# Performance work log

Hardware: AMD Instinct MI355X
Metric: run time of the kernel (lower is better)

The kernel has to match this reference:

```python
import jax, jax.numpy as jnp
import numpy as np

SPEED_OF_SOUND = 343.0
SAMPLING_FREQUENCY = 96000.0
REC_LEN = 4096   # recording_length_samples
CROP_LEN = 128   # crop_length_samples
NUM_RECV = 8
B1, B2 = 4, 16384
HIDDEN = 32


def setup_inputs() -> dict:
    key = jax.random.key(0)
    ks = jax.random.split(key, 6)
    recordings = jax.random.normal(ks[0], (B1, NUM_RECV, REC_LEN), dtype=jnp.float32)
    sample_locations = jax.random.normal(ks[1], (B1, B2, 3), dtype=jnp.float32)
    emitter_location = jax.random.normal(ks[2], (3,), dtype=jnp.float32)
    receiver_locations = jax.random.normal(ks[3], (NUM_RECV, 3), dtype=jnp.float32)
    W1 = 0.02 * jax.random.normal(ks[4], (NUM_RECV * CROP_LEN, HIDDEN), dtype=jnp.float32)
    b1 = jnp.zeros((HIDDEN,), dtype=jnp.float32)
    W2 = 0.02 * jax.random.normal(ks[5], (HIDDEN, 1), dtype=jnp.float32)
    b2 = jnp.zeros((1,), dtype=jnp.float32)
    return {
        "recordings": recordings,
        "sample_locations": sample_locations,
        "emitter_location": emitter_location,
        "receiver_locations": receiver_locations,
        "W1": W1, "b1": b1, "W2": W2, "b2": b2,
    }


def reference(recordings, sample_locations, emitter_location, receiver_locations, W1, b1, W2, b2):
    # recordings: (B1, R, L); sample_locations: (B1, B2, 3)
    b1_, R, L = recordings.shape
    b2_ = sample_locations.shape[1]
    K = W1.shape[0] // R  # crop_length_samples

    # time-of-flight distances
    d_emit = jnp.linalg.norm(sample_locations - emitter_location, axis=-1)              # (B1, B2)
    d_recv = jnp.linalg.norm(sample_locations[:, :, None, :] - receiver_locations, axis=-1)  # (B1, B2, R)
    total_samples = jnp.round((d_emit[..., None] + d_recv) / SPEED_OF_SOUND * SAMPLING_FREQUENCY)
    crop_start = total_samples - K // 2                                                  # (B1, B2, R)

    # normalized grid coordinates, exactly as in the torch module
    grid_base = -1.0 + 2.0 * (crop_start / L)                                            # (B1, B2, R)
    grid_offset = jnp.linspace(0.0, 0.5 * (K - 1) / L, K, dtype=jnp.float32)             # (K,)
    gx = grid_base[..., None] + grid_offset                                              # (B1, B2, R, K)

    # Exact torch grid_sample(mode='bilinear', align_corners=False, zero padding) on
    # input of shape (N, 1, H=L, W=1) with grid = (x=gx, y=0). In torch, x indexes the
    # WIDTH dim (size 1) and y=0 indexes the HEIGHT dim (size L), so:
    #   iy = ((0+1)*L - 1)/2 = (L-1)/2  (constant -> blend of the two center samples)
    #   ix = ((gx+1)*1 - 1)/2 = gx/2    (triangle weight around the single width pixel)
    iy = (L - 1) / 2.0
    iy0 = int(np.floor(iy))
    wy1 = jnp.float32(iy - iy0)
    wy0 = jnp.float32(1.0) - wy1
    vy = wy0 * recordings[..., iy0] + wy1 * recordings[..., iy0 + 1]                     # (B1, R)

    ix = gx * 0.5
    ix0 = jnp.floor(ix)
    fx = ix - ix0
    # corner at width index ix0 is in-bounds iff ix0 == 0; corner ix0+1 iff ix0 == -1
    w = (1.0 - fx) * (ix0 == 0.0).astype(ix.dtype) + fx * (ix0 == -1.0).astype(ix.dtype)
    crops = w * vy[:, None, :, None]                                                     # (B1, B2, R, K)

    # tiny MLP head
    x = crops.reshape(b1_ * b2_, R * K)
    h = jax.nn.relu(x @ W1 + b1)
    pred = (h @ W2 + b2).reshape(b1_, b2_)
    return pred
```

## Files before the change

### kernel.cpp

```cpp
#include <hip/hip_runtime.h>
#include <math.h>

#define TMAX 6336
#define B2N  16384

__global__ __launch_bounds__(256) void build_S(const float* __restrict__ W1,
                                               float* __restrict__ S) {
  const int r  = blockIdx.y;
  const int T0 = blockIdx.x * 64;
  __shared__ float W1s[128 * 32];
  __shared__ float wls[128 * 64];
  const int t = threadIdx.x;

  const float4* src = (const float4*)(W1 + r * 128 * 32);
  float4* dst = (float4*)W1s;
#pragma unroll
  for (int i = 0; i < 4; i++) dst[t + i * 256] = src[t + i * 256];

  for (int e = t; e < 128 * 64; e += 256) {
    const int k  = e >> 6;
    const int Tl = e & 63;
    const float g0 = (float)(T0 + Tl - 64) * (1.0f / 2048.0f) - 1.0f;
    const float gx = g0 + (float)k * (1.0f / 8192.0f);
    wls[e] = fmaxf(0.0f, fmaf(-0.5f, fabsf(gx), 1.0f));
  }
  __syncthreads();

  const int h  = t & 31;
  const int tb = t >> 5;
  float acc[8] = {0.f, 0.f, 0.f, 0.f, 0.f, 0.f, 0.f, 0.f};
#pragma unroll 4
  for (int k = 0; k < 128; k++) {
    const float wv = W1s[k * 32 + h];
    const float4* wp = (const float4*)(&wls[k * 64 + tb * 8]);
    const float4 w0 = wp[0];
    const float4 w1 = wp[1];
    acc[0] = fmaf(w0.x, wv, acc[0]);
    acc[1] = fmaf(w0.y, wv, acc[1]);
    acc[2] = fmaf(w0.z, wv, acc[2]);
    acc[3] = fmaf(w0.w, wv, acc[3]);
    acc[4] = fmaf(w1.x, wv, acc[4]);
    acc[5] = fmaf(w1.y, wv, acc[5]);
    acc[6] = fmaf(w1.z, wv, acc[6]);
    acc[7] = fmaf(w1.w, wv, acc[7]);
  }
#pragma unroll
  for (int j = 0; j < 8; j++) {
    const int T = T0 + tb * 8 + j;
    S[(((T << 3) + r) << 5) + h] = acc[j];
  }
}

__global__ __launch_bounds__(256) void tof_main(
    const float* __restrict__ recordings, const float* __restrict__ sloc,
    const float* __restrict__ emit, const float* __restrict__ rloc,
    const float* __restrict__ b1v, const float* __restrict__ W2,
    const float* __restrict__ b2v, const float* __restrict__ S,
    float* __restrict__ out) {
  __shared__ float vy[8];
  __shared__ float em[3];
  __shared__ float rl[24];
  __shared__ float b1s[32];
  __shared__ float W2s[32];
  __shared__ float b2s;
  const int t = threadIdx.x;
  const int sid = blockIdx.x * 256 + t;
  const int b = sid >> 14;

  if (t < 8) {
    const float* rp = recordings + ((b << 3) + t) * 4096;
    vy[t] = 0.5f * (rp[2047] + rp[2048]);
  }
  if (t < 3) em[t] = emit[t];
  if (t >= 32 && t < 56) rl[t - 32] = rloc[t - 32];
  if (t >= 64 && t < 96) b1s[t - 64] = b1v[t - 64];
  if (t >= 96 && t < 128) W2s[t - 96] = W2[t - 96];
  if (t == 128) b2s = b2v[0];
  __syncthreads();

  const float x = sloc[sid * 3 + 0];
  const float y = sloc[sid * 3 + 1];
  const float z = sloc[sid * 3 + 2];
  const float ex = x - em[0], ey = y - em[1], ez = z - em[2];
  const float de = sqrtf(ex * ex + ey * ey + ez * ez);

  float acc[32];
#pragma unroll
  for (int h = 0; h < 32; h++) acc[h] = 0.f;

#pragma unroll
  for (int r = 0; r < 8; r++) {
    const float rx = x - rl[r * 3 + 0];
    const float ry = y - rl[r * 3 + 1];
    const float rz = z - rl[r * 3 + 2];
    const float dr = sqrtf(rx * rx + ry * ry + rz * rz);
    const float ts = rintf(((de + dr) / 343.0f) * 96000.0f);
    int T = (int)ts;
    T = min(max(T, 0), TMAX - 1);
    const float4* Srow = (const float4*)(S + (((T << 3) + r) << 5));
    const float vr = vy[r];
#pragma unroll
    for (int q = 0; q < 8; q++) {
      const float4 v = Srow[q];
      acc[4 * q + 0] = fmaf(vr, v.x, acc[4 * q + 0]);
      acc[4 * q + 1] = fmaf(vr, v.y, acc[4 * q + 1]);
      acc[4 * q + 2] = fmaf(vr, v.z, acc[4 * q + 2]);
      acc[4 * q + 3] = fmaf(vr, v.w, acc[4 * q + 3]);
    }
  }

  float pred = b2s;
#pragma unroll
  for (int h = 0; h < 32; h++) {
    const float hv = fmaxf(acc[h] + b1s[h], 0.0f);
    pred = fmaf(hv, W2s[h], pred);
  }
  out[sid] = pred;
}

__global__ __launch_bounds__(256) void tof_fused(
    const float* __restrict__ recordings, const float* __restrict__ sloc,
    const float* __restrict__ emit, const float* __restrict__ rloc,
    const float* __restrict__ W1, const float* __restrict__ b1v,
    const float* __restrict__ W2, const float* __restrict__ b2v,
    float* __restrict__ out) {
  __shared__ float vy[8];
  __shared__ float em[3];
  __shared__ float rl[24];
  __shared__ float b1s[32];
  __shared__ float W2s[32];
  __shared__ float b2s;
  const int t = threadIdx.x;
  const int sid = blockIdx.x * 256 + t;
  const int b = sid >> 14;

  if (t < 8) {
    const float* rp = recordings + ((b << 3) + t) * 4096;
    vy[t] = 0.5f * (rp[2047] + rp[2048]);
  }
  if (t < 3) em[t] = emit[t];
  if (t >= 32 && t < 56) rl[t - 32] = rloc[t - 32];
  if (t >= 64 && t < 96) b1s[t - 64] = b1v[t - 64];
  if (t >= 96 && t < 128) W2s[t - 96] = W2[t - 96];
  if (t == 128) b2s = b2v[0];
  __syncthreads();

  const float x = sloc[sid * 3 + 0];
  const float y = sloc[sid * 3 + 1];
  const float z = sloc[sid * 3 + 2];
  const float ex = x - em[0], ey = y - em[1], ez = z - em[2];
  const float de = sqrtf(ex * ex + ey * ey + ez * ez);

  float acc[32];
#pragma unroll
  for (int h = 0; h < 32; h++) acc[h] = 0.f;

  for (int r = 0; r < 8; r++) {
    const float rx = x - rl[r * 3 + 0];
    const float ry = y - rl[r * 3 + 1];
    const float rz = z - rl[r * 3 + 2];
    const float dr = sqrtf(rx * rx + ry * ry + rz * rz);
    const float ts = rintf(((de + dr) / 343.0f) * 96000.0f);
    const float g0 = ts * (1.0f / 2048.0f) - (1.0f + 64.0f / 2048.0f);
    const float vr = vy[r];
    for (int k = 0; k < 128; k++) {
      const float gx = g0 + (float)k * (1.0f / 8192.0f);
      const float w = fmaxf(0.0f, fmaf(-0.5f, fabsf(gx), 1.0f));
      const float c = w * vr;
      const float* wrow = W1 + (((r << 7) + k) << 5);
#pragma unroll
      for (int h = 0; h < 32; h++) acc[h] = fmaf(c, wrow[h], acc[h]);
    }
  }

  float pred = b2s;
#pragma unroll
  for (int h = 0; h < 32; h++) {
    const float hv = fmaxf(acc[h] + b1s[h], 0.0f);
    pred = fmaf(hv, W2s[h], pred);
  }
  out[sid] = pred;
}

extern "C" void kernel_launch(void* const* d_in, const int* in_sizes, int n_in,
                              void* d_out, int out_size, void* d_ws,
                              size_t ws_size, hipStream_t stream) {
  const float* recordings = (const float*)d_in[0];
  const float* sloc       = (const float*)d_in[1];
  const float* emit       = (const float*)d_in[2];
  const float* rloc       = (const float*)d_in[3];
  const float* W1         = (const float*)d_in[4];
  const float* b1v        = (const float*)d_in[5];
  const float* W2         = (const float*)d_in[6];
  const float* b2v        = (const float*)d_in[7];
  float* out = (float*)d_out;

  const size_t s_bytes = (size_t)TMAX * 8 * 32 * sizeof(float);
  if (ws_size >= s_bytes) {
    float* S = (float*)d_ws;
    dim3 g1(TMAX / 64, 8);
    build_S<<<g1, 256, 0, stream>>>(W1, S);
    tof_main<<<256, 256, 0, stream>>>(recordings, sloc, emit, rloc, b1v, W2,
                                      b2v, S, out);
  } else {
    tof_fused<<<256, 256, 0, stream>>>(recordings, sloc, emit, rloc, W1, b1v,
                                       W2, b2v, out);
  }
}
```

Measured before the change: 95.03 us.

## Replace per-T lookup table with prefix sums of W1 exploiting piecewise-linear weights

The crop weights are a piecewise-linear triangle in k, so the W1 contraction can be written through prefix sums P (sum of W1 rows) and Q (k-weighted sum) over k. The large TMAX x 8 x 32 table build_S used to fill is replaced by a small prep kernel that computes these prefix arrays. The main kernel then uses the totals kept in shared memory for samples whose crop lies entirely on one side of the kink, and gathers at two breakpoints only when the crop straddles it. This removes most of the precompute work and the scattered global gathers, at the cost of a serial 128-step scan in prep and some change in floating-point rounding.

New measurement: 82.15 us. 13.5% less time.

```diff
diff --git a/kernel.cpp b/kernel.cpp
--- a/kernel.cpp
+++ b/kernel.cpp
@@ -1,53 +1,32 @@
 #include <hip/hip_runtime.h>
 #include <math.h>
 
-#define TMAX 6336
-#define B2N  16384
-
-__global__ __launch_bounds__(256) void build_S(const float* __restrict__ W1,
-                                               float* __restrict__ S) {
-  const int r  = blockIdx.y;
-  const int T0 = blockIdx.x * 64;
-  __shared__ float W1s[128 * 32];
-  __shared__ float wls[128 * 64];
+#define PQ_STRIDE (129 * 256)
+
+__global__ __launch_bounds__(256) void prep(const float* __restrict__ W1,
+                                            float* __restrict__ P,
+                                            float* __restrict__ Q) {
+  __shared__ float slab[2 * 128 * 32];
   const int t = threadIdx.x;
-
-  const float4* src = (const float4*)(W1 + r * 128 * 32);
-  float4* dst = (float4*)W1s;
-#pragma unroll
-  for (int i = 0; i < 4; i++) dst[t + i * 256] = src[t + i * 256];
-
-  for (int e = t; e < 128 * 64; e += 256) {
-    const int k  = e >> 6;
-    const int Tl = e & 63;
-    const float g0 = (float)(T0 + Tl - 64) * (1.0f / 2048.0f) - 1.0f;
-    const float gx = g0 + (float)k * (1.0f / 8192.0f);
-    wls[e] = fmaxf(0.0f, fmaf(-0.5f, fabsf(gx), 1.0f));
-  }
+  const int r0 = blockIdx.x * 2;
+  const float4* src = (const float4*)(W1 + r0 * 128 * 32);
+  float4* dst = (float4*)slab;
+#pragma unroll
+  for (int i = 0; i < 8; i++) dst[t + i * 256] = src[t + i * 256];
   __syncthreads();
-
-  const int h  = t & 31;
-  const int tb = t >> 5;
-  float acc[8] = {0.f, 0.f, 0.f, 0.f, 0.f, 0.f, 0.f, 0.f};
-#pragma unroll 4
-  for (int k = 0; k < 128; k++) {
-    const float wv = W1s[k * 32 + h];
-    const float4* wp = (const float4*)(&wls[k * 64 + tb * 8]);
-    const float4 w0 = wp[0];
-    const float4 w1 = wp[1];
-    acc[0] = fmaf(w0.x, wv, acc[0]);
-    acc[1] = fmaf(w0.y, wv, acc[1]);
-    acc[2] = fmaf(w0.z, wv, acc[2]);
-    acc[3] = fmaf(w0.w, wv, acc[3]);
-    acc[4] = fmaf(w1.x, wv, acc[4]);
-    acc[5] = fmaf(w1.y, wv, acc[5]);
-    acc[6] = fmaf(w1.z, wv, acc[6]);
-    acc[7] = fmaf(w1.w, wv, acc[7]);
-  }
-#pragma unroll
-  for (int j = 0; j < 8; j++) {
-    const int T = T0 + tb * 8 + j;
-    S[(((T << 3) + r) << 5) + h] = acc[j];
+  if (t < 64) {
+    const int rl = t >> 5, h = t & 31;
+    const int r = r0 + rl;
+    float p = 0.f, q = 0.f;
+    for (int k = 0; k < 128; k++) {
+      P[k * 256 + r * 32 + h] = p;
+      Q[k * 256 + r * 32 + h] = q;
+      const float w = slab[(rl * 128 + k) * 32 + h];
+      p += w;
+      q = fmaf((float)k * (1.0f / 16384.0f), w, q);
+    }
+    P[128 * 256 + r * 32 + h] = p;
+    Q[128 * 256 + r * 32 + h] = q;
   }
 }
 
@@ -55,65 +34,113 @@
     const float* __restrict__ recordings, const float* __restrict__ sloc,
     const float* __restrict__ emit, const float* __restrict__ rloc,
     const float* __restrict__ b1v, const float* __restrict__ W2,
-    const float* __restrict__ b2v, const float* __restrict__ S,
-    float* __restrict__ out) {
-  __shared__ float vy[8];
-  __shared__ float em[3];
-  __shared__ float rl[24];
-  __shared__ float b1s[32];
-  __shared__ float W2s[32];
+    const float* __restrict__ b2v, const float* __restrict__ Pg,
+    const float* __restrict__ Qg, float* __restrict__ out) {
+  __shared__ __align__(16) float Ps[256];
+  __shared__ __align__(16) float Qs[256];
+  __shared__ __align__(16) float b1s[32];
+  __shared__ __align__(16) float W2s[32];
+  __shared__ float vys[8];
+  __shared__ float ems[3];
+  __shared__ float rls[24];
   __shared__ float b2s;
   const int t = threadIdx.x;
   const int sid = blockIdx.x * 256 + t;
   const int b = sid >> 14;
 
-  if (t < 8) {
-    const float* rp = recordings + ((b << 3) + t) * 4096;
-    vy[t] = 0.5f * (rp[2047] + rp[2048]);
-  }
-  if (t < 3) em[t] = emit[t];
-  if (t >= 32 && t < 56) rl[t - 32] = rloc[t - 32];
-  if (t >= 64 && t < 96) b1s[t - 64] = b1v[t - 64];
-  if (t >= 96 && t < 128) W2s[t - 96] = W2[t - 96];
-  if (t == 128) b2s = b2v[0];
+  if (t < 64) {
+    ((float4*)Ps)[t] = ((const float4*)(Pg + 128 * 256))[t];
+  } else if (t < 128) {
+    ((float4*)Qs)[t - 64] = ((const float4*)(Qg + 128 * 256))[t - 64];
+  } else if (t < 152) {
+    rls[t - 128] = rloc[t - 128];
+  } else if (t < 155) {
+    ems[t - 152] = emit[t - 152];
+  } else if (t == 155) {
+    b2s = b2v[0];
+  } else if (t >= 160 && t < 168) {
+    const int r = t - 160;
+    const float* rp = recordings + ((b << 3) + r) * 4096;
+    vys[r] = 0.5f * (rp[2047] + rp[2048]);
+  } else if (t >= 192 && t < 224) {
+    b1s[t - 192] = b1v[t - 192];
+  } else if (t >= 224) {
+    W2s[t - 224] = W2[t - 224];
+  }
   __syncthreads();
 
-  const float x = sloc[sid * 3 + 0];
-  const float y = sloc[sid * 3 + 1];
-  const float z = sloc[sid * 3 + 2];
-  const float ex = x - em[0], ey = y - em[1], ez = z - em[2];
+  const float xx = sloc[3 * sid + 0];
+  const float yy = sloc[3 * sid + 1];
+  const float zz = sloc[3 * sid + 2];
+  const float ex = xx - ems[0], ey = yy - ems[1], ez = zz - ems[2];
   const float de = sqrtf(ex * ex + ey * ey + ez * ez);
 
-  float acc[32];
-#pragma unroll
-  for (int h = 0; h < 32; h++) acc[h] = 0.f;
+  float4 acc[8];
+#pragma unroll
+  for (int q = 0; q < 8; q++) acc[q] = make_float4(0.f, 0.f, 0.f, 0.f);
 
 #pragma unroll
   for (int r = 0; r < 8; r++) {
-    const float rx = x - rl[r * 3 + 0];
-    const float ry = y - rl[r * 3 + 1];
-    const float rz = z - rl[r * 3 + 2];
+    const float rx = xx - rls[3 * r + 0];
+    const float ry = yy - rls[3 * r + 1];
+    const float rz = zz - rls[3 * r + 2];
     const float dr = sqrtf(rx * rx + ry * ry + rz * rz);
     const float ts = rintf(((de + dr) / 343.0f) * 96000.0f);
-    int T = (int)ts;
-    T = min(max(T, 0), TMAX - 1);
-    const float4* Srow = (const float4*)(S + (((T << 3) + r) << 5));
-    const float vr = vy[r];
-#pragma unroll
-    for (int q = 0; q < 8; q++) {
-      const float4 v = Srow[q];
-      acc[4 * q + 0] = fmaf(vr, v.x, acc[4 * q + 0]);
-      acc[4 * q + 1] = fmaf(vr, v.y, acc[4 * q + 1]);
-      acc[4 * q + 2] = fmaf(vr, v.z, acc[4 * q + 2]);
-      acc[4 * q + 3] = fmaf(vr, v.w, acc[4 * q + 3]);
+    const int T = (int)ts;
+    const float g0 = (ts - 64.0f) * (1.0f / 2048.0f) - 1.0f;
+    const float vr = vys[r];
+    const bool fast1 = (T <= 2080);
+    const bool fast3 = (T >= 2112) && (T <= 6176);
+    if (fast1 | fast3) {
+      const float sg = fast1 ? 1.0f : -1.0f;
+      const float aa = vr * fmaf(0.5f * sg, g0, 1.0f);
+      const float cc = sg * vr;
+      const float4* Pr = (const float4*)(Ps + r * 32);
+      const float4* Qr = (const float4*)(Qs + r * 32);
+#pragma unroll
+      for (int q = 0; q < 8; q++) {
+        const float4 pv = Pr[q];
+        const float4 qv = Qr[q];
+        acc[q].x = fmaf(aa, pv.x, fmaf(cc, qv.x, acc[q].x));
+        acc[q].y = fmaf(aa, pv.y, fmaf(cc, qv.y, acc[q].y));
+        acc[q].z = fmaf(aa, pv.z, fmaf(cc, qv.z, acc[q].z));
+        acc[q].w = fmaf(aa, pv.w, fmaf(cc, qv.w, acc[q].w));
+      }
+    } else {
+      int ka = 8448 - 4 * T;  ka = min(max(ka, 0), 128);
+      int kb = 24832 - 4 * T; kb = min(max(kb, 0), 128);
+      const float u = fmaf(0.5f, g0, 1.0f);
+      const float v = fmaf(-0.5f, g0, 1.0f);
+      const float4* Pa = (const float4*)(Pg + ka * 256 + r * 32);
+      const float4* Qa = (const float4*)(Qg + ka * 256 + r * 32);
+      const float4* Pb = (const float4*)(Pg + kb * 256 + r * 32);
+      const float4* Qb = (const float4*)(Qg + kb * 256 + r * 32);
+#pragma unroll
+      for (int q = 0; q < 8; q++) {
+        const float4 pa = Pa[q], qa = Qa[q], pb = Pb[q], qb = Qb[q];
+        const float s0 = u * pa.x + qa.x + v * (pb.x - pa.x) - (qb.x - qa.x);
+        const float s1 = u * pa.y + qa.y + v * (pb.y - pa.y) - (qb.y - qa.y);
+        const float s2 = u * pa.z + qa.z + v * (pb.z - pa.z) - (qb.z - qa.z);
+        const float s3 = u * pa.w + qa.w + v * (pb.w - pa.w) - (qb.w - qa.w);
+        acc[q].x = fmaf(vr, s0, acc[q].x);
+        acc[q].y = fmaf(vr, s1, acc[q].y);
+        acc[q].z = fmaf(vr, s2, acc[q].z);
+        acc[q].w = fmaf(vr, s3, acc[q].w);
+      }
     }
   }
 
   float pred = b2s;
-#pragma unroll
-  for (int h = 0; h < 32; h++) {
-    const float hv = fmaxf(acc[h] + b1s[h], 0.0f);
-    pred = fmaf(hv, W2s[h], pred);
+  const float4* b14 = (const float4*)b1s;
+  const float4* W24 = (const float4*)W2s;
+#pragma unroll
+  for (int q = 0; q < 8; q++) {
+    const float4 hb = b14[q];
+    const float4 wv = W24[q];
+    pred = fmaf(fmaxf(acc[q].x + hb.x, 0.0f), wv.x, pred);
+    pred = fmaf(fmaxf(acc[q].y + hb.y, 0.0f), wv.y, pred);
+    pred = fmaf(fmaxf(acc[q].z + hb.z, 0.0f), wv.z, pred);
+    pred = fmaf(fmaxf(acc[q].w + hb.w, 0.0f), wv.w, pred);
   }
   out[sid] = pred;
 }
@@ -195,13 +222,13 @@
   const float* b2v        = (const float*)d_in[7];
   float* out = (float*)d_out;
 
-  const size_t s_bytes = (size_t)TMAX * 8 * 32 * sizeof(float);
-  if (ws_size >= s_bytes) {
-    float* S = (float*)d_ws;
-    dim3 g1(TMAX / 64, 8);
-    build_S<<<g1, 256, 0, stream>>>(W1, S);
+  const size_t pq_bytes = (size_t)2 * PQ_STRIDE * sizeof(float);
+  if (ws_size >= pq_bytes) {
+    float* P = (float*)d_ws;
+    float* Q = P + PQ_STRIDE;
+    prep<<<4, 256, 0, stream>>>(W1, P, Q);
     tof_main<<<256, 256, 0, stream>>>(recordings, sloc, emit, rloc, b1v, W2,
-                                      b2v, S, out);
+                                      b2v, P, Q, out);
   } else {
     tof_fused<<<256, 256, 0, stream>>>(recordings, sloc, emit, rloc, W1, b1v,
                                        W2, b2v, out);
```
